# Kernel optimization log

Measured on AMD Instinct MI355X. Metric: run time of the kernel, lower is better.

## Reference

```python
import jax, jax.numpy as jnp
import numpy as np

N, E, IN, HID, HEADS, L = 50000, 640000, 32, 64, 2, 4
MAXR = 8
N_ETYPE = 11 + 3 * MAXR  # 35
NEG_SLOPE = 0.2  # DGL EGATConv leaky_relu slope


def _mlp2(x, W1, b1, W2, b2):
    # 2-layer MLP: activation (gelu) after hidden layer only
    return jax.nn.gelu(x @ W1 + b1) @ W2 + b2


def _egat(h, ef, src, dst, W_ni, W_nj, W_fij, W_node, b_node, attn):
    # DGL EGATConv: edge-feature-enhanced graph attention
    n = h.shape[0]
    H, D = attn.shape
    f_edge = (h @ W_ni)[src] + (h @ W_nj)[dst] + ef @ W_fij       # [E, H*D]
    f_out = jax.nn.leaky_relu(f_edge, NEG_SLOPE).reshape(-1, H, D)
    e = jnp.einsum('ehd,hd->eh', f_out, attn)                     # [E, H]
    m = jax.ops.segment_max(e, dst, num_segments=n)               # per-dst max
    w = jnp.exp(e - m[dst])
    z = jax.ops.segment_sum(w, dst, num_segments=n)
    a = w / z[dst]                                                # edge softmax over incoming edges
    h_out = (h @ W_node + b_node).reshape(n, H, D)
    return jax.ops.segment_sum(h_out[src] * a[:, :, None], dst, num_segments=n)  # [N, H, D]


def _forward(feat, att_rc, att_rp, type_emb, rid_emb, rc_W, rc_b, rp_W, rp_b,
             fe_W1, fe_b1, fe_W2, fe_b2, W_ni, W_nj, W_fij, W_node, b_node, attn,
             mlp_W1, mlp_b1, mlp_W2, mlp_b2, src, dst, etype, erid):
    n = feat.shape[0]
    # edge embedding, 'sum' flavor
    ef = type_emb[etype] + rid_emb[erid] + att_rc @ rc_W + rc_b + att_rp @ rp_W + rp_b
    feats = [feat]
    h = _mlp2(feat, fe_W1, fe_b1, fe_W2, fe_b2)
    feats.append(h)
    for l in range(W_ni.shape[0]):
        agg = _egat(h, ef, src, dst, W_ni[l], W_nj[l], W_fij[l],
                    W_node[l], b_node[l], attn[l])
        h = _mlp2(agg.reshape(n, -1), mlp_W1[l], mlp_b1[l], mlp_W2[l], mlp_b2[l]) + h  # residual
        feats.append(h)
    node_emb = jnp.concatenate(feats, axis=-1)             # layer_pooling='all'
    graph_emb = jnp.max(node_emb, axis=0, keepdims=True)   # graph max pooling
    return jnp.concatenate([node_emb, jnp.broadcast_to(graph_emb, node_emb.shape)], axis=-1)


def setup_inputs() -> dict:
    key = jax.random.key(0)
    ks = iter(jax.random.split(key, 40))
    s = 0.05
    return {
        'feat': jax.random.normal(next(ks), (N, IN), jnp.float32),
        'att_rc': jax.random.normal(next(ks), (E, 2), jnp.float32),
        'att_rp': jax.random.normal(next(ks), (E, 3), jnp.float32),
        'type_emb': jax.random.normal(next(ks), (N_ETYPE, HID), jnp.float32) * s,
        'rid_emb': jax.random.normal(next(ks), (MAXR + 1, HID), jnp.float32) * s,
        'rc_W': jax.random.normal(next(ks), (2, HID), jnp.float32) * s,
        'rc_b': jnp.zeros((HID,), jnp.float32),
        'rp_W': jax.random.normal(next(ks), (3, HID), jnp.float32) * s,
        'rp_b': jnp.zeros((HID,), jnp.float32),
        'fe_W1': jax.random.normal(next(ks), (IN, HID), jnp.float32) * s,
        'fe_b1': jnp.zeros((HID,), jnp.float32),
        'fe_W2': jax.random.normal(next(ks), (HID, HID), jnp.float32) * s,
        'fe_b2': jnp.zeros((HID,), jnp.float32),
        'W_ni': jax.random.normal(next(ks), (L, HID, HEADS * HID), jnp.float32) * s,
        'W_nj': jax.random.normal(next(ks), (L, HID, HEADS * HID), jnp.float32) * s,
        'W_fij': jax.random.normal(next(ks), (L, HID, HEADS * HID), jnp.float32) * s,
        'W_node': jax.random.normal(next(ks), (L, HID, HEADS * HID), jnp.float32) * s,
        'b_node': jnp.zeros((L, HEADS * HID), jnp.float32),
        'attn': jax.random.normal(next(ks), (L, HEADS, HID), jnp.float32) * s,
        'mlp_W1': jax.random.normal(next(ks), (L, HEADS * HID, HEADS * HID), jnp.float32) * s,
        'mlp_b1': jnp.zeros((L, HEADS * HID), jnp.float32),
        'mlp_W2': jax.random.normal(next(ks), (L, HEADS * HID, HID), jnp.float32) * s,
        'mlp_b2': jnp.zeros((L, HID), jnp.float32),
        'src': jax.random.randint(next(ks), (E,), 0, N, jnp.int32),
        'dst': jax.random.randint(next(ks), (E,), 0, N, jnp.int32),
        'etype': jax.random.randint(next(ks), (E,), 0, N_ETYPE, jnp.int32),
        'erid': jax.random.randint(next(ks), (E,), 0, MAXR + 1, jnp.int32),
    }


def reference(feat, att_rc, att_rp, type_emb, rid_emb, rc_W, rc_b, rp_W, rp_b,
              fe_W1, fe_b1, fe_W2, fe_b2, W_ni, W_nj, W_fij, W_node, b_node, attn,
              mlp_W1, mlp_b1, mlp_W2, mlp_b2, src, dst, etype, erid):
    return _forward(feat, att_rc, att_rp, type_emb, rid_emb, rc_W, rc_b, rp_W, rp_b,
                    fe_W1, fe_b1, fe_W2, fe_b2, W_ni, W_nj, W_fij, W_node, b_node, attn,
                    mlp_W1, mlp_b1, mlp_W2, mlp_b2, src, dst, etype, erid)
```

## Files before the change

kernel.cpp:

```cpp
#include <hip/hip_runtime.h>
#include <math.h>

#define N_NODES 50000
#define N_EDGES 640000
#define NLAYER  4
#define NPAD    50016

typedef unsigned short bf16_t;
typedef __attribute__((ext_vector_type(8))) short s16x8;
typedef __attribute__((ext_vector_type(4))) float f32x4;

__device__ __forceinline__ float gelu_f(float x) {
    return 0.5f * x * (1.0f + tanhf(0.7978845608028654f * (x + 0.044715f * x * x * x)));
}

__device__ __forceinline__ bf16_t f2bf(float f) {
    unsigned u = __float_as_uint(f);
    unsigned r = (u + 0x7FFFu + ((u >> 16) & 1u)) >> 16;
    return (bf16_t)r;
}
__device__ __forceinline__ float bf2f(bf16_t h) { return __uint_as_float(((unsigned)h) << 16); }
__device__ __forceinline__ float bfl(unsigned x) { return __uint_as_float(x << 16); }
__device__ __forceinline__ float bfh(unsigned x) { return __uint_as_float(x & 0xFFFF0000u); }

__global__ void k_zero32(unsigned* p, int n) {
    int i = blockIdx.x * 256 + threadIdx.x;
    if (i < n) p[i] = 0u;
}

__global__ void k_hist(const int* __restrict__ dst, int* __restrict__ deg) {
    int i = blockIdx.x * 256 + threadIdx.x;
    if (i < N_EDGES) atomicAdd(&deg[dst[i]], 1);
}

__global__ void k_scan1(const int* __restrict__ deg, int* __restrict__ rowptr, int* __restrict__ bsum) {
    __shared__ int sd[1024];
    int gi = blockIdx.x * 1024 + threadIdx.x;
    int v = (gi < N_NODES) ? deg[gi] : 0;
    sd[threadIdx.x] = v;
    __syncthreads();
    for (int off = 1; off < 1024; off <<= 1) {
        int t2 = (threadIdx.x >= (unsigned)off) ? sd[threadIdx.x - off] : 0;
        __syncthreads();
        sd[threadIdx.x] += t2;
        __syncthreads();
    }
    if (gi < N_NODES) rowptr[gi] = sd[threadIdx.x] - v;
    if (threadIdx.x == 1023) bsum[blockIdx.x] = sd[1023];
}

__global__ void k_scan2(const int* __restrict__ bsum, int* __restrict__ boff, int nb) {
    if (threadIdx.x == 0 && blockIdx.x == 0) {
        int run = 0;
        for (int b = 0; b < nb; b++) { boff[b] = run; run += bsum[b]; }
    }
}

__global__ void k_scan3(int* __restrict__ rowptr, const int* __restrict__ boff) {
    int gi = blockIdx.x * 1024 + threadIdx.x;
    if (gi < N_NODES) rowptr[gi] += boff[blockIdx.x];
    if (gi == 0) rowptr[N_NODES] = N_EDGES;
}

__global__ void k_copy(const int* __restrict__ a, int* __restrict__ b) {
    int i = blockIdx.x * 256 + threadIdx.x;
    if (i < N_NODES) b[i] = a[i];
}

__global__ void k_scatter(const int* __restrict__ dst, int* __restrict__ cursor, int* __restrict__ eidx) {
    int i = blockIdx.x * 256 + threadIdx.x;
    if (i < N_EDGES) {
        int p = atomicAdd(&cursor[dst[i]], 1);
        eidx[p] = i;
    }
}

__global__ void k_sortgather(
    const int* __restrict__ eidx, const int* __restrict__ src, const int* __restrict__ dst,
    const int* __restrict__ etype, const int* __restrict__ erid,
    const float* __restrict__ att_rc, const float* __restrict__ att_rp,
    int* __restrict__ src_s, int* __restrict__ dst_s,
    int* __restrict__ etype_s, int* __restrict__ erid_s,
    float* __restrict__ rc_s, float* __restrict__ rp_s)
{
    int i = blockIdx.x * 256 + threadIdx.x;
    if (i < N_EDGES) {
        int e = eidx[i];
        src_s[i] = src[e];
        dst_s[i] = dst[e];
        etype_s[i] = etype[e];
        erid_s[i] = erid[e];
        rc_s[2 * i] = att_rc[2 * e];
        rc_s[2 * i + 1] = att_rc[2 * e + 1];
        rp_s[3 * i] = att_rp[3 * e];
        rp_s[3 * i + 1] = att_rp[3 * e + 1];
        rp_s[3 * i + 2] = att_rp[3 * e + 2];
    }
}

__global__ void k_wprep(const float* __restrict__ Wfij, const float* __restrict__ Wni,
                        const float* __restrict__ Wnj, const float* __restrict__ Wnode,
                        const float* __restrict__ W1, const float* __restrict__ W2,
                        bf16_t* __restrict__ WT, bf16_t* __restrict__ W3T,
                        bf16_t* __restrict__ W1T, bf16_t* __restrict__ W2T)
{
    int idx = blockIdx.x * 256 + threadIdx.x;
    if (idx >= NLAYER * 57344) return;
    int l = idx / 57344, r = idx % 57344;
    if (r < 8192) {
        int n = r >> 6, k = r & 63;
        WT[l * 8192 + r] = f2bf(Wfij[l * 8192 + k * 128 + n]);
    } else if (r < 32768) {
        int q = r - 8192; int c = q >> 6, k = q & 63;
        const float* src = (c < 128) ? Wni : (c < 256) ? Wnj : Wnode;
        W3T[l * 24576 + q] = f2bf(src[l * 8192 + k * 128 + (c & 127)]);
    } else if (r < 49152) {
        int q = r - 32768; int n = q >> 7, k = q & 127;
        W1T[l * 16384 + q] = f2bf(W1[l * 16384 + k * 128 + n]);
    } else {
        int q = r - 49152; int j = q >> 7, k = q & 127;
        W2T[l * 8192 + q] = f2bf(W2[l * 8192 + k * 64 + j]);
    }
}

__global__ __launch_bounds__(256) void k_fe(
    const float* __restrict__ feat, const float* __restrict__ W1, const float* __restrict__ b1,
    const float* __restrict__ W2, const float* __restrict__ b2,
    float* __restrict__ h, bf16_t* __restrict__ hb, float* __restrict__ out)
{
    __shared__ float hid[4][64];
    int w = threadIdx.x >> 6, lane = threadIdx.x & 63;
    int n = blockIdx.x * 4 + w;
    float a = b1[lane];
#pragma unroll 8
    for (int k = 0; k < 32; k++) a = fmaf(feat[n * 32 + k], W1[k * 64 + lane], a);
    hid[w][lane] = gelu_f(a);
    __syncthreads();
    float o = b2[lane];
#pragma unroll 8
    for (int k = 0; k < 64; k++) o = fmaf(hid[w][k], W2[k * 64 + lane], o);
    h[n * 64 + lane] = o;
    hb[n * 64 + lane] = f2bf(o);
    out[n * 704 + 32 + lane] = o;
    if (lane < 32) out[n * 704 + lane] = feat[n * 32 + lane];
}

__global__ __launch_bounds__(256) void k_node3(
    const bf16_t* __restrict__ hb, const bf16_t* __restrict__ W3T,
    const float* __restrict__ bnode, bf16_t* __restrict__ s)
{
    __shared__ __align__(16) bf16_t hbS[32 * 72];
    const int t = threadIdx.x;
    const int wave = t >> 6, lane = t & 63, l16 = lane & 15, quad = lane >> 4;
    const int n0 = blockIdx.x * 32;
    {
        int r = t >> 3, sg = t & 7;
        *(s16x8*)(hbS + r * 72 + sg * 8) = *(const s16x8*)(hb + (size_t)(n0 + r) * 64 + sg * 8);
    }
    __syncthreads();
    const int ng = wave & 1, ch = wave >> 1;
    const s16x8 B0 = *(const s16x8*)(hbS + (ng * 16 + l16) * 72 + quad * 8);
    const s16x8 B1 = *(const s16x8*)(hbS + (ng * 16 + l16) * 72 + 32 + quad * 8);
    const int node = n0 + ng * 16 + l16;
#pragma unroll
    for (int nt = 0; nt < 12; nt++) {
        int c0 = ch * 192 + nt * 16;
        const s16x8 A0 = *(const s16x8*)(W3T + (size_t)(c0 + l16) * 64 + quad * 8);
        const s16x8 A1 = *(const s16x8*)(W3T + (size_t)(c0 + l16) * 64 + 32 + quad * 8);
        f32x4 acc = {0.f, 0.f, 0.f, 0.f};
        acc = __builtin_amdgcn_mfma_f32_16x16x32_bf16(A0, B0, acc, 0, 0, 0);
        acc = __builtin_amdgcn_mfma_f32_16x16x32_bf16(A1, B1, acc, 0, 0, 0);
        int cb = c0 + quad * 4;
        float4 bv = make_float4(0.f, 0.f, 0.f, 0.f);
        if (cb >= 256) bv = *(const float4*)(bnode + cb - 256);
        ushort4 o;
        o.x = f2bf(acc[0] + bv.x);
        o.y = f2bf(acc[1] + bv.y);
        o.z = f2bf(acc[2] + bv.z);
        o.w = f2bf(acc[3] + bv.w);
        *(ushort4*)(s + (size_t)node * 384 + cb) = o;
    }
}

__global__ __launch_bounds__(256) void k_edge(
    const bf16_t* __restrict__ s, const bf16_t* __restrict__ WT,
    const float* __restrict__ attn,
    const float* __restrict__ type_emb, const float* __restrict__ rid_emb,
    const float* __restrict__ rcW, const float* __restrict__ rcb,
    const float* __restrict__ rpW, const float* __restrict__ rpb,
    const float* __restrict__ rc_s, const float* __restrict__ rp_s,
    const int* __restrict__ etype_s, const int* __restrict__ erid_s,
    const int* __restrict__ src_s, const int* __restrict__ dst_s,
    float* __restrict__ evals)
{
    __shared__ __align__(16) bf16_t efA[32 * 72];
    __shared__ __align__(16) bf16_t SND[32 * 136];
    const int t = threadIdx.x;
    const int wave = t >> 6, lane = t & 63;
    const int l16 = lane & 15, quad = lane >> 4;
    const int eg = wave & 1, head = wave >> 1;

    s16x8 Aw[4][2];
    float4 att4[4];
#pragma unroll
    for (int mt = 0; mt < 4; mt++) {
        const bf16_t* wrow = WT + (head * 64 + mt * 16 + l16) * 64 + quad * 8;
        Aw[mt][0] = *(const s16x8*)(wrow);
        Aw[mt][1] = *(const s16x8*)(wrow + 32);
        att4[mt] = *(const float4*)(attn + head * 64 + mt * 16 + quad * 4);
    }

    for (int tile = blockIdx.x; tile < N_EDGES / 32; tile += gridDim.x) {
        const int eb = tile * 32;
        __syncthreads();
        {
            int e = t & 31, kg = (t >> 5) * 8;
            int i = eb + e;
            int et = etype_s[i] * 64, er = erid_s[i] * 64;
            float rc0 = rc_s[i * 2 + 0], rc1 = rc_s[i * 2 + 1];
            float rp0 = rp_s[i * 3 + 0], rp1 = rp_s[i * 3 + 1], rp2 = rp_s[i * 3 + 2];
            bf16_t tmp[8];
#pragma unroll
            for (int kk = 0; kk < 8; kk++) {
                int k = kg + kk;
                float v = type_emb[et + k] + rid_emb[er + k] + rcb[k] + rpb[k];
                v = fmaf(rc0, rcW[k], v);
                v = fmaf(rc1, rcW[64 + k], v);
                v = fmaf(rp0, rpW[k], v);
                v = fmaf(rp1, rpW[64 + k], v);
                v = fmaf(rp2, rpW[128 + k], v);
                tmp[kk] = f2bf(v);
            }
            *(s16x8*)(&efA[e * 72 + kg]) = *(const s16x8*)tmp;
        }
        {
#pragma unroll
            for (int j = 0; j < 2; j++) {
                int c = t * 2 + j;
                int e = c >> 4, p = c & 15;
                int i = eb + e;
                const uint4 U = *(const uint4*)(s + (size_t)src_s[i] * 384 + p * 8);
                const uint4 V = *(const uint4*)(s + (size_t)dst_s[i] * 384 + 128 + p * 8);
                bf16_t o[8];
                o[0] = f2bf(bfl(U.x) + bfl(V.x)); o[1] = f2bf(bfh(U.x) + bfh(V.x));
                o[2] = f2bf(bfl(U.y) + bfl(V.y)); o[3] = f2bf(bfh(U.y) + bfh(V.y));
                o[4] = f2bf(bfl(U.z) + bfl(V.z)); o[5] = f2bf(bfh(U.z) + bfh(V.z));
                o[6] = f2bf(bfl(U.w) + bfl(V.w)); o[7] = f2bf(bfh(U.w) + bfh(V.w));
                *(s16x8*)(&SND[e * 136 + p * 8]) = *(const s16x8*)o;
            }
        }
        __syncthreads();

        const int e = eg * 16 + l16;
        const s16x8 B0 = *(const s16x8*)(&efA[e * 72 + quad * 8]);
        const s16x8 B1 = *(const s16x8*)(&efA[e * 72 + 32 + quad * 8]);
        f32x4 acc[4];
#pragma unroll
        for (int mt = 0; mt < 4; mt++) {
            f32x4 a = {0.f, 0.f, 0.f, 0.f};
            a = __builtin_amdgcn_mfma_f32_16x16x32_bf16(Aw[mt][0], B0, a, 0, 0, 0);
            a = __builtin_amdgcn_mfma_f32_16x16x32_bf16(Aw[mt][1], B1, a, 0, 0, 0);
            acc[mt] = a;
        }

        float p = 0.f;
#pragma unroll
        for (int mt = 0; mt < 4; mt++) {
            const ushort4 sv = *(const ushort4*)(&SND[e * 136 + mt * 16 + quad * 4]);
            float f0 = acc[mt][0] + bf2f(sv.x);
            float f1 = acc[mt][1] + bf2f(sv.y);
            float f2 = acc[mt][2] + bf2f(sv.z);
            float f3 = acc[mt][3] + bf2f(sv.w);
            f0 = (f0 >= 0.f) ? f0 : 0.2f * f0;
            f1 = (f1 >= 0.f) ? f1 : 0.2f * f1;
            f2 = (f2 >= 0.f) ? f2 : 0.2f * f2;
            f3 = (f3 >= 0.f) ? f3 : 0.2f * f3;
            p = fmaf(f0, att4[mt].x, p);
            p = fmaf(f1, att4[mt].y, p);
            p = fmaf(f2, att4[mt].z, p);
            p = fmaf(f3, att4[mt].w, p);
        }
        p += __shfl_xor(p, 16);
        p += __shfl_xor(p, 32);
        if (quad == 0) evals[(eb + e) * 2 + head] = p;
    }
}

__global__ __launch_bounds__(256) void k_soft_agg(
    const int* __restrict__ rowptr, const int* __restrict__ src_s,
    const float* __restrict__ evals, const bf16_t* __restrict__ s,
    unsigned* __restrict__ aggb)
{
    int lane = threadIdx.x & 63;
    int wid = (blockIdx.x * 256 + threadIdx.x) >> 6;
    int nw = (gridDim.x * 256) >> 6;
    const int h1 = (lane >= 32) ? 1 : 0;
    const int half = lane & 31;
    for (int n = wid; n < N_NODES; n += nw) {
        int r0 = rowptr[n], r1 = rowptr[n + 1];
        unsigned* aout = aggb + (size_t)n * 64 + lane;
        if (r0 == r1) { *aout = 0u; continue; }
        float mm = -1e30f;
        for (int i = r0 + half; i < r1; i += 32) mm = fmaxf(mm, evals[2 * i + h1]);
#pragma unroll
        for (int off = 1; off < 32; off <<= 1) mm = fmaxf(mm, __shfl_xor(mm, off));
        float z = 0.f;
        for (int i = r0 + half; i < r1; i += 32) z += expf(evals[2 * i + h1] - mm);
#pragma unroll
        for (int off = 1; off < 32; off <<= 1) z += __shfl_xor(z, off);
        float rz = 1.f / z;
        float acc0 = 0.f, acc1 = 0.f;
        for (int i = r0; i < r1; i += 8) {
            int cnt = r1 - i;
            unsigned cc[8]; float ww[8];
#pragma unroll
            for (int j = 0; j < 8; j++) {
                if (j < cnt) {
                    cc[j] = *(const unsigned*)(s + (size_t)src_s[i + j] * 384 + 256 + 2 * lane);
                    ww[j] = expf(evals[2 * (i + j) + h1] - mm) * rz;
                } else { cc[j] = 0u; ww[j] = 0.f; }
            }
#pragma unroll
            for (int j = 0; j < 8; j++) {
                acc0 = fmaf(ww[j], bfl(cc[j]), acc0);
                acc1 = fmaf(ww[j], bfh(cc[j]), acc1);
            }
        }
        *aout = (unsigned)f2bf(acc0) | ((unsigned)f2bf(acc1) << 16);
    }
}

__global__ __launch_bounds__(256) void k_mlp(
    const bf16_t* __restrict__ aggb, const bf16_t* __restrict__ W1T, const float* __restrict__ b1,
    const bf16_t* __restrict__ W2T, const float* __restrict__ b2,
    const float* __restrict__ hin, float* __restrict__ hout, bf16_t* __restrict__ houtb,
    float* __restrict__ out, int col0)
{
    __shared__ __align__(16) bf16_t aggS[32 * 136];
    __shared__ __align__(16) bf16_t hidS[32 * 136];
    const int t = threadIdx.x;
    const int wave = t >> 6, lane = t & 63, l16 = lane & 15, quad = lane >> 4;
    const int n0 = blockIdx.x * 32;
    {
        int r = t >> 3, sg = t & 7;
        *(s16x8*)(aggS + r * 136 + sg * 16) =
            *(const s16x8*)(aggb + (size_t)(n0 + r) * 128 + sg * 16);
        *(s16x8*)(aggS + r * 136 + sg * 16 + 8) =
            *(const s16x8*)(aggb + (size_t)(n0 + r) * 128 + sg * 16 + 8);
    }
    __syncthreads();
    const int ng = wave & 1, nh = wave >> 1;
    const int node = n0 + ng * 16 + l16;
    {
        const bf16_t* brow = aggS + (ng * 16 + l16) * 136 + quad * 8;
        s16x8 B[4];
#pragma unroll
        for (int ks = 0; ks < 4; ks++) B[ks] = *(const s16x8*)(brow + ks * 32);
#pragma unroll
        for (int nt = 0; nt < 4; nt++) {
            int nb = nh * 64 + nt * 16;
            f32x4 acc = {0.f, 0.f, 0.f, 0.f};
#pragma unroll
            for (int ks = 0; ks < 4; ks++) {
                const s16x8 A = *(const s16x8*)(W1T + (size_t)(nb + l16) * 128 + ks * 32 + quad * 8);
                acc = __builtin_amdgcn_mfma_f32_16x16x32_bf16(A, B[ks], acc, 0, 0, 0);
            }
            const float4 bv = *(const float4*)(b1 + nb + quad * 4);
            ushort4 o;
            o.x = f2bf(gelu_f(acc[0] + bv.x));
            o.y = f2bf(gelu_f(acc[1] + bv.y));
            o.z = f2bf(gelu_f(acc[2] + bv.z));
            o.w = f2bf(gelu_f(acc[3] + bv.w));
            *(ushort4*)(hidS + (ng * 16 + l16) * 136 + nb + quad * 4) = o;
        }
    }
    __syncthreads();
    {
        const int jh = wave >> 1;
        const bf16_t* hrow = hidS + (ng * 16 + l16) * 136 + quad * 8;
        s16x8 H[4];
#pragma unroll
        for (int ks = 0; ks < 4; ks++) H[ks] = *(const s16x8*)(hrow + ks * 32);
#pragma unroll
        for (int jt = 0; jt < 2; jt++) {
            int jb = jh * 32 + jt * 16;
            f32x4 acc = {0.f, 0.f, 0.f, 0.f};
#pragma unroll
            for (int ks = 0; ks < 4; ks++) {
                const s16x8 A = *(const s16x8*)(W2T + (size_t)(jb + l16) * 128 + ks * 32 + quad * 8);
                acc = __builtin_amdgcn_mfma_f32_16x16x32_bf16(A, H[ks], acc, 0, 0, 0);
            }
            int j0 = jb + quad * 4;
            const float4 bv = *(const float4*)(b2 + j0);
            const float4 hv = *(const float4*)(hin + (size_t)node * 64 + j0);
            float4 v;
            v.x = acc[0] + bv.x + hv.x;
            v.y = acc[1] + bv.y + hv.y;
            v.z = acc[2] + bv.z + hv.z;
            v.w = acc[3] + bv.w + hv.w;
            *(float4*)(hout + (size_t)node * 64 + j0) = v;
            ushort4 ob;
            ob.x = f2bf(v.x); ob.y = f2bf(v.y); ob.z = f2bf(v.z); ob.w = f2bf(v.w);
            *(ushort4*)(houtb + (size_t)node * 64 + j0) = ob;
            if (node < N_NODES)
                *(float4*)(out + (size_t)node * 704 + col0 + j0) = v;
        }
    }
}

__device__ __forceinline__ unsigned fmap(float v) {
    unsigned u = __float_as_uint(v);
    return (u & 0x80000000u) ? ~u : (u | 0x80000000u);
}

__global__ __launch_bounds__(384) void k_colmax(const float* __restrict__ out, unsigned* __restrict__ gmax) {
    int c = threadIdx.x;
    if (c >= 352) return;
    float m = -1e30f;
    for (int n = blockIdx.x; n < N_NODES; n += gridDim.x)
        m = fmaxf(m, out[(size_t)n * 704 + c]);
    atomicMax(gmax + c, fmap(m));
}

__global__ __launch_bounds__(384) void k_bcast(const unsigned* __restrict__ gmax, float* __restrict__ out) {
    int c = threadIdx.x;
    if (c >= 352) return;
    unsigned u = gmax[c];
    u = (u & 0x80000000u) ? (u ^ 0x80000000u) : ~u;
    float v = __uint_as_float(u);
    for (int n = blockIdx.x; n < N_NODES; n += gridDim.x)
        out[(size_t)n * 704 + 352 + c] = v;
}

extern "C" void kernel_launch(void* const* d_in, const int* in_sizes, int n_in,
                              void* d_out, int out_size, void* d_ws, size_t ws_size,
                              hipStream_t stream)
{
    (void)in_sizes; (void)n_in; (void)out_size; (void)ws_size;
    const float* feat     = (const float*)d_in[0];
    const float* att_rc   = (const float*)d_in[1];
    const float* att_rp   = (const float*)d_in[2];
    const float* type_emb = (const float*)d_in[3];
    const float* rid_emb  = (const float*)d_in[4];
    const float* rc_W     = (const float*)d_in[5];
    const float* rc_b     = (const float*)d_in[6];
    const float* rp_W     = (const float*)d_in[7];
    const float* rp_b     = (const float*)d_in[8];
    const float* fe_W1    = (const float*)d_in[9];
    const float* fe_b1    = (const float*)d_in[10];
    const float* fe_W2    = (const float*)d_in[11];
    const float* fe_b2    = (const float*)d_in[12];
    const float* W_ni     = (const float*)d_in[13];
    const float* W_nj     = (const float*)d_in[14];
    const float* W_fij    = (const float*)d_in[15];
    const float* W_node   = (const float*)d_in[16];
    const float* b_node   = (const float*)d_in[17];
    const float* attn     = (const float*)d_in[18];
    const float* mlp_W1   = (const float*)d_in[19];
    const float* mlp_b1   = (const float*)d_in[20];
    const float* mlp_W2   = (const float*)d_in[21];
    const float* mlp_b2   = (const float*)d_in[22];
    const int* src   = (const int*)d_in[23];
    const int* dst   = (const int*)d_in[24];
    const int* etype = (const int*)d_in[25];
    const int* erid  = (const int*)d_in[26];
    float* out = (float*)d_out;

    char* cur = (char*)d_ws;
    auto alloc = [&](size_t bytes) { char* p = cur; cur += (bytes + 15) & ~(size_t)15; return p; };
    float* h_a    = (float*)alloc((size_t)NPAD * 64 * 4);
    float* h_b    = (float*)alloc((size_t)NPAD * 64 * 4);
    bf16_t* hb_a  = (bf16_t*)alloc((size_t)NPAD * 64 * 2);
    bf16_t* hb_b  = (bf16_t*)alloc((size_t)NPAD * 64 * 2);
    bf16_t* s     = (bf16_t*)alloc((size_t)NPAD * 384 * 2);
    float* ev     = (float*)alloc((size_t)N_EDGES * 2 * 4);
    bf16_t* aggb  = (bf16_t*)alloc((size_t)NPAD * 128 * 2);
    int* deg     = (int*)alloc((size_t)N_NODES * 4);
    int* rowptr  = (int*)alloc((size_t)(N_NODES + 1) * 4);
    int* cursor  = (int*)alloc((size_t)N_NODES * 4);
    int* eidx    = (int*)alloc((size_t)N_EDGES * 4);
    int* src_s   = (int*)alloc((size_t)N_EDGES * 4);
    int* dst_s   = (int*)alloc((size_t)N_EDGES * 4);
    int* etype_s = (int*)alloc((size_t)N_EDGES * 4);
    int* erid_s  = (int*)alloc((size_t)N_EDGES * 4);
    float* rc_s  = (float*)alloc((size_t)N_EDGES * 2 * 4);
    float* rp_s  = (float*)alloc((size_t)N_EDGES * 3 * 4);
    bf16_t* WT   = (bf16_t*)alloc((size_t)NLAYER * 128 * 64 * 2);
    bf16_t* W3T  = (bf16_t*)alloc((size_t)NLAYER * 384 * 64 * 2);
    bf16_t* W1T  = (bf16_t*)alloc((size_t)NLAYER * 128 * 128 * 2);
    bf16_t* W2T  = (bf16_t*)alloc((size_t)NLAYER * 64 * 128 * 2);
    int* bsum    = (int*)alloc(64 * 4);
    int* boff    = (int*)alloc(64 * 4);
    unsigned* gmax = (unsigned*)alloc(352 * 4);

    const int NB = (N_NODES + 1023) / 1024;

    k_zero32<<<(N_NODES + 255) / 256, 256, 0, stream>>>((unsigned*)deg, N_NODES);
    k_zero32<<<2, 256, 0, stream>>>(gmax, 352);
    k_hist<<<N_EDGES / 256, 256, 0, stream>>>(dst, deg);
    k_scan1<<<NB, 1024, 0, stream>>>(deg, rowptr, bsum);
    k_scan2<<<1, 64, 0, stream>>>(bsum, boff, NB);
    k_scan3<<<NB, 1024, 0, stream>>>(rowptr, boff);
    k_copy<<<(N_NODES + 255) / 256, 256, 0, stream>>>(rowptr, cursor);
    k_scatter<<<N_EDGES / 256, 256, 0, stream>>>(dst, cursor, eidx);
    k_sortgather<<<N_EDGES / 256, 256, 0, stream>>>(eidx, src, dst, etype, erid, att_rc, att_rp,
                                                    src_s, dst_s, etype_s, erid_s, rc_s, rp_s);
    k_wprep<<<(NLAYER * 57344 + 255) / 256, 256, 0, stream>>>(
        W_fij, W_ni, W_nj, W_node, mlp_W1, mlp_W2, WT, W3T, W1T, W2T);
    k_fe<<<N_NODES / 4, 256, 0, stream>>>(feat, fe_W1, fe_b1, fe_W2, fe_b2, h_a, hb_a, out);

    float* hc = h_a;  bf16_t* hbc = hb_a;
    float* hn = h_b;  bf16_t* hbn = hb_b;
    for (int l = 0; l < NLAYER; l++) {
        k_node3<<<NPAD / 32, 256, 0, stream>>>(hbc, W3T + (size_t)l * 384 * 64, b_node + l * 128, s);
        k_edge<<<2560, 256, 0, stream>>>(s, WT + l * 128 * 64, attn + l * 128,
                                         type_emb, rid_emb, rc_W, rc_b, rp_W, rp_b,
                                         rc_s, rp_s, etype_s, erid_s, src_s, dst_s, ev);
        k_soft_agg<<<4096, 256, 0, stream>>>(rowptr, src_s, ev, s, (unsigned*)aggb);
        k_mlp<<<NPAD / 32, 256, 0, stream>>>(aggb, W1T + (size_t)l * 128 * 128, mlp_b1 + l * 128,
                                             W2T + (size_t)l * 64 * 128, mlp_b2 + l * 64,
                                             hc, hn, hbn, out, 32 + 64 * (l + 1));
        float* tf = hc; hc = hn; hn = tf;
        bf16_t* tb = hbc; hbc = hbn; hbn = tb;
    }
    k_colmax<<<512, 384, 0, stream>>>(out, gmax);
    k_bcast<<<512, 384, 0, stream>>>(gmax, out);
}
```

Baseline: 1.330 ms.

## Restructure edge kernel to per-wave tiles with packed edge metadata and base table

Packs per-edge metadata (combined type/rid index, src, dst, rc/rp attributes) into a 32-byte record so the edge kernel does two vector loads per edge instead of many scattered ones. Precomputes a 315x64 table of type+rid embeddings plus biases, which removes two embedding lookups and bias adds per edge. The edge kernel now has each wave process 16 edges for both heads directly from registers, with weights staged once in LDS, removing per-tile block barriers and the LDS round trips. This raises register pressure (both heads' weight fragments held in registers) and each wave's gathers of node rows are narrower.

```diff
diff --git a/kernel.cpp b/kernel.cpp
--- a/kernel.cpp
+++ b/kernel.cpp
@@ -79,23 +79,36 @@
     const int* __restrict__ eidx, const int* __restrict__ src, const int* __restrict__ dst,
     const int* __restrict__ etype, const int* __restrict__ erid,
     const float* __restrict__ att_rc, const float* __restrict__ att_rp,
-    int* __restrict__ src_s, int* __restrict__ dst_s,
-    int* __restrict__ etype_s, int* __restrict__ erid_s,
-    float* __restrict__ rc_s, float* __restrict__ rp_s)
+    int* __restrict__ src_s, uint4* __restrict__ emeta)
 {
     int i = blockIdx.x * 256 + threadIdx.x;
     if (i < N_EDGES) {
         int e = eidx[i];
-        src_s[i] = src[e];
-        dst_s[i] = dst[e];
-        etype_s[i] = etype[e];
-        erid_s[i] = erid[e];
-        rc_s[2 * i] = att_rc[2 * e];
-        rc_s[2 * i + 1] = att_rc[2 * e + 1];
-        rp_s[3 * i] = att_rp[3 * e];
-        rp_s[3 * i + 1] = att_rp[3 * e + 1];
-        rp_s[3 * i + 2] = att_rp[3 * e + 2];
-    }
+        int sv = src[e];
+        src_s[i] = sv;
+        uint4 a, b;
+        a.x = (unsigned)(etype[e] * 9 + erid[e]);
+        a.y = (unsigned)sv;
+        a.z = (unsigned)dst[e];
+        a.w = __float_as_uint(att_rc[2 * e]);
+        b.x = __float_as_uint(att_rc[2 * e + 1]);
+        b.y = __float_as_uint(att_rp[3 * e]);
+        b.z = __float_as_uint(att_rp[3 * e + 1]);
+        b.w = __float_as_uint(att_rp[3 * e + 2]);
+        emeta[2 * i] = a;
+        emeta[2 * i + 1] = b;
+    }
+}
+
+__global__ void k_base(const float* __restrict__ type_emb, const float* __restrict__ rid_emb,
+                       const float* __restrict__ rcb, const float* __restrict__ rpb,
+                       float* __restrict__ base)
+{
+    int idx = blockIdx.x * 256 + threadIdx.x;
+    if (idx >= 315 * 64) return;
+    int c = idx >> 6, k = idx & 63;
+    int et = c / 9, er = c % 9;
+    base[idx] = type_emb[et * 64 + k] + rid_emb[er * 64 + k] + rcb[k] + rpb[k];
 }
 
 __global__ void k_wprep(const float* __restrict__ Wfij, const float* __restrict__ Wni,
@@ -184,105 +197,123 @@
 
 __global__ __launch_bounds__(256) void k_edge(
     const bf16_t* __restrict__ s, const bf16_t* __restrict__ WT,
-    const float* __restrict__ attn,
-    const float* __restrict__ type_emb, const float* __restrict__ rid_emb,
-    const float* __restrict__ rcW, const float* __restrict__ rcb,
-    const float* __restrict__ rpW, const float* __restrict__ rpb,
-    const float* __restrict__ rc_s, const float* __restrict__ rp_s,
-    const int* __restrict__ etype_s, const int* __restrict__ erid_s,
-    const int* __restrict__ src_s, const int* __restrict__ dst_s,
-    float* __restrict__ evals)
-{
-    __shared__ __align__(16) bf16_t efA[32 * 72];
-    __shared__ __align__(16) bf16_t SND[32 * 136];
-    const int t = threadIdx.x;
-    const int wave = t >> 6, lane = t & 63;
+    const float* __restrict__ attn, const uint4* __restrict__ emeta,
+    const float* __restrict__ base, const float* __restrict__ rcW,
+    const float* __restrict__ rpW, float* __restrict__ evals)
+{
+    __shared__ __align__(16) bf16_t WTl[128 * 72];
+    __shared__ __align__(16) float attL[128];
+    __shared__ __align__(16) float cwL[5][64];
+    for (int c = threadIdx.x; c < 1024; c += 256) {
+        int r = c >> 3, q = c & 7;
+        *(s16x8*)(WTl + r * 72 + q * 8) = *(const s16x8*)(WT + r * 64 + q * 8);
+    }
+    if (threadIdx.x < 128) attL[threadIdx.x] = attn[threadIdx.x];
+    {
+        int j = threadIdx.x >> 6, k = threadIdx.x & 63;
+        cwL[j][k] = (j < 2) ? rcW[j * 64 + k] : rpW[(j - 2) * 64 + k];
+        if (threadIdx.x < 64) cwL[4][threadIdx.x] = rpW[128 + threadIdx.x];
+    }
+    __syncthreads();
+
+    const int lane = threadIdx.x & 63;
     const int l16 = lane & 15, quad = lane >> 4;
-    const int eg = wave & 1, head = wave >> 1;
-
-    s16x8 Aw[4][2];
-    float4 att4[4];
-#pragma unroll
-    for (int mt = 0; mt < 4; mt++) {
-        const bf16_t* wrow = WT + (head * 64 + mt * 16 + l16) * 64 + quad * 8;
-        Aw[mt][0] = *(const s16x8*)(wrow);
-        Aw[mt][1] = *(const s16x8*)(wrow + 32);
-        att4[mt] = *(const float4*)(attn + head * 64 + mt * 16 + quad * 4);
-    }
-
-    for (int tile = blockIdx.x; tile < N_EDGES / 32; tile += gridDim.x) {
-        const int eb = tile * 32;
-        __syncthreads();
-        {
-            int e = t & 31, kg = (t >> 5) * 8;
-            int i = eb + e;
-            int et = etype_s[i] * 64, er = erid_s[i] * 64;
-            float rc0 = rc_s[i * 2 + 0], rc1 = rc_s[i * 2 + 1];
-            float rp0 = rp_s[i * 3 + 0], rp1 = rp_s[i * 3 + 1], rp2 = rp_s[i * 3 + 2];
-            bf16_t tmp[8];
-#pragma unroll
-            for (int kk = 0; kk < 8; kk++) {
-                int k = kg + kk;
-                float v = type_emb[et + k] + rid_emb[er + k] + rcb[k] + rpb[k];
-                v = fmaf(rc0, rcW[k], v);
-                v = fmaf(rc1, rcW[64 + k], v);
-                v = fmaf(rp0, rpW[k], v);
-                v = fmaf(rp1, rpW[64 + k], v);
-                v = fmaf(rp2, rpW[128 + k], v);
-                tmp[kk] = f2bf(v);
+
+    s16x8 Aw[2][4][2];
+#pragma unroll
+    for (int hd = 0; hd < 2; hd++)
+#pragma unroll
+        for (int mt = 0; mt < 4; mt++) {
+            const bf16_t* arow = WTl + (hd * 64 + mt * 16 + l16) * 72 + quad * 8;
+            Aw[hd][mt][0] = *(const s16x8*)(arow);
+            Aw[hd][mt][1] = *(const s16x8*)(arow + 32);
+        }
+
+    const int nw = (gridDim.x * 256) >> 6;
+    for (int tile = (blockIdx.x * 256 + threadIdx.x) >> 6; tile < N_EDGES / 16; tile += nw) {
+        const int i = tile * 16 + l16;
+        const uint4 m0 = emeta[2 * i];
+        const uint4 m1 = emeta[2 * i + 1];
+
+        const bf16_t* srow = s + (size_t)m0.y * 384;
+        const bf16_t* drow = s + (size_t)m0.z * 384 + 128;
+        ushort4 niv[4], njv[4];
+#pragma unroll
+        for (int mt = 0; mt < 4; mt++) {
+            const int d0 = mt * 16 + quad * 4;
+            niv[mt] = *(const ushort4*)(srow + d0);
+            njv[mt] = *(const ushort4*)(drow + d0);
+        }
+
+        const float* bp = base + (size_t)m0.x * 64;
+        const float4 bv0 = *(const float4*)(bp + quad * 8);
+        const float4 bv1 = *(const float4*)(bp + quad * 8 + 4);
+        const float4 bv2 = *(const float4*)(bp + 32 + quad * 8);
+        const float4 bv3 = *(const float4*)(bp + 32 + quad * 8 + 4);
+        const float rc0 = __uint_as_float(m0.w), rc1 = __uint_as_float(m1.x);
+        const float rp0 = __uint_as_float(m1.y), rp1 = __uint_as_float(m1.z), rp2 = __uint_as_float(m1.w);
+
+        auto efg = [&](const float4& bv, int k) -> ushort4 {
+            const float4 w0 = *(const float4*)(&cwL[0][k]);
+            const float4 w1 = *(const float4*)(&cwL[1][k]);
+            const float4 w2 = *(const float4*)(&cwL[2][k]);
+            const float4 w3 = *(const float4*)(&cwL[3][k]);
+            const float4 w4 = *(const float4*)(&cwL[4][k]);
+            float v0 = bv.x, v1 = bv.y, v2 = bv.z, v3 = bv.w;
+            v0 = fmaf(rc0, w0.x, v0); v1 = fmaf(rc0, w0.y, v1); v2 = fmaf(rc0, w0.z, v2); v3 = fmaf(rc0, w0.w, v3);
+            v0 = fmaf(rc1, w1.x, v0); v1 = fmaf(rc1, w1.y, v1); v2 = fmaf(rc1, w1.z, v2); v3 = fmaf(rc1, w1.w, v3);
+            v0 = fmaf(rp0, w2.x, v0); v1 = fmaf(rp0, w2.y, v1); v2 = fmaf(rp0, w2.z, v2); v3 = fmaf(rp0, w2.w, v3);
+            v0 = fmaf(rp1, w3.x, v0); v1 = fmaf(rp1, w3.y, v1); v2 = fmaf(rp1, w3.z, v2); v3 = fmaf(rp1, w3.w, v3);
+            v0 = fmaf(rp2, w4.x, v0); v1 = fmaf(rp2, w4.y, v1); v2 = fmaf(rp2, w4.z, v2); v3 = fmaf(rp2, w4.w, v3);
+            ushort4 r;
+            r.x = f2bf(v0); r.y = f2bf(v1); r.z = f2bf(v2); r.w = f2bf(v3);
+            return r;
+        };
+        const ushort4 e0 = efg(bv0, quad * 8);
+        const ushort4 e1 = efg(bv1, quad * 8 + 4);
+        const ushort4 e2 = efg(bv2, 32 + quad * 8);
+        const ushort4 e3 = efg(bv3, 32 + quad * 8 + 4);
+        s16x8 B0, B1;
+        B0[0] = (short)e0.x; B0[1] = (short)e0.y; B0[2] = (short)e0.z; B0[3] = (short)e0.w;
+        B0[4] = (short)e1.x; B0[5] = (short)e1.y; B0[6] = (short)e1.z; B0[7] = (short)e1.w;
+        B1[0] = (short)e2.x; B1[1] = (short)e2.y; B1[2] = (short)e2.z; B1[3] = (short)e2.w;
+        B1[4] = (short)e3.x; B1[5] = (short)e3.y; B1[6] = (short)e3.z; B1[7] = (short)e3.w;
+
+        ushort4 snd[4];
+#pragma unroll
+        for (int mt = 0; mt < 4; mt++) {
+            snd[mt].x = f2bf(bf2f(niv[mt].x) + bf2f(njv[mt].x));
+            snd[mt].y = f2bf(bf2f(niv[mt].y) + bf2f(njv[mt].y));
+            snd[mt].z = f2bf(bf2f(niv[mt].z) + bf2f(njv[mt].z));
+            snd[mt].w = f2bf(bf2f(niv[mt].w) + bf2f(njv[mt].w));
+        }
+
+#pragma unroll
+        for (int hd = 0; hd < 2; hd++) {
+            float p = 0.f;
+#pragma unroll
+            for (int mt = 0; mt < 4; mt++) {
+                f32x4 a = {0.f, 0.f, 0.f, 0.f};
+                a = __builtin_amdgcn_mfma_f32_16x16x32_bf16(Aw[hd][mt][0], B0, a, 0, 0, 0);
+                a = __builtin_amdgcn_mfma_f32_16x16x32_bf16(Aw[hd][mt][1], B1, a, 0, 0, 0);
+                const float4 at = *(const float4*)(attL + hd * 64 + mt * 16 + quad * 4);
+                float f0 = a[0] + bf2f(snd[mt].x);
+                float f1 = a[1] + bf2f(snd[mt].y);
+                float f2 = a[2] + bf2f(snd[mt].z);
+                float f3 = a[3] + bf2f(snd[mt].w);
+                f0 = (f0 >= 0.f) ? f0 : 0.2f * f0;
+                f1 = (f1 >= 0.f) ? f1 : 0.2f * f1;
+                f2 = (f2 >= 0.f) ? f2 : 0.2f * f2;
+                f3 = (f3 >= 0.f) ? f3 : 0.2f * f3;
+                p = fmaf(f0, at.x, p);
+                p = fmaf(f1, at.y, p);
+                p = fmaf(f2, at.z, p);
+                p = fmaf(f3, at.w, p);
             }
-            *(s16x8*)(&efA[e * 72 + kg]) = *(const s16x8*)tmp;
-        }
-        {
-#pragma unroll
-            for (int j = 0; j < 2; j++) {
-                int c = t * 2 + j;
-                int e = c >> 4, p = c & 15;
-                int i = eb + e;
-                const uint4 U = *(const uint4*)(s + (size_t)src_s[i] * 384 + p * 8);
-                const uint4 V = *(const uint4*)(s + (size_t)dst_s[i] * 384 + 128 + p * 8);
-                bf16_t o[8];
-                o[0] = f2bf(bfl(U.x) + bfl(V.x)); o[1] = f2bf(bfh(U.x) + bfh(V.x));
-                o[2] = f2bf(bfl(U.y) + bfl(V.y)); o[3] = f2bf(bfh(U.y) + bfh(V.y));
-                o[4] = f2bf(bfl(U.z) + bfl(V.z)); o[5] = f2bf(bfh(U.z) + bfh(V.z));
-                o[6] = f2bf(bfl(U.w) + bfl(V.w)); o[7] = f2bf(bfh(U.w) + bfh(V.w));
-                *(s16x8*)(&SND[e * 136 + p * 8]) = *(const s16x8*)o;
-            }
-        }
-        __syncthreads();
-
-        const int e = eg * 16 + l16;
-        const s16x8 B0 = *(const s16x8*)(&efA[e * 72 + quad * 8]);
-        const s16x8 B1 = *(const s16x8*)(&efA[e * 72 + 32 + quad * 8]);
-        f32x4 acc[4];
-#pragma unroll
-        for (int mt = 0; mt < 4; mt++) {
-            f32x4 a = {0.f, 0.f, 0.f, 0.f};
-            a = __builtin_amdgcn_mfma_f32_16x16x32_bf16(Aw[mt][0], B0, a, 0, 0, 0);
-            a = __builtin_amdgcn_mfma_f32_16x16x32_bf16(Aw[mt][1], B1, a, 0, 0, 0);
-            acc[mt] = a;
-        }
-
-        float p = 0.f;
-#pragma unroll
-        for (int mt = 0; mt < 4; mt++) {
-            const ushort4 sv = *(const ushort4*)(&SND[e * 136 + mt * 16 + quad * 4]);
-            float f0 = acc[mt][0] + bf2f(sv.x);
-            float f1 = acc[mt][1] + bf2f(sv.y);
-            float f2 = acc[mt][2] + bf2f(sv.z);
-            float f3 = acc[mt][3] + bf2f(sv.w);
-            f0 = (f0 >= 0.f) ? f0 : 0.2f * f0;
-            f1 = (f1 >= 0.f) ? f1 : 0.2f * f1;
-            f2 = (f2 >= 0.f) ? f2 : 0.2f * f2;
-            f3 = (f3 >= 0.f) ? f3 : 0.2f * f3;
-            p = fmaf(f0, att4[mt].x, p);
-            p = fmaf(f1, att4[mt].y, p);
-            p = fmaf(f2, att4[mt].z, p);
-            p = fmaf(f3, att4[mt].w, p);
-        }
-        p += __shfl_xor(p, 16);
-        p += __shfl_xor(p, 32);
-        if (quad == 0) evals[(eb + e) * 2 + head] = p;
+            p += __shfl_xor(p, 16);
+            p += __shfl_xor(p, 32);
+            if (quad == 0) evals[i * 2 + hd] = p;
+        }
     }
 }
 
@@ -480,11 +511,8 @@
     int* cursor  = (int*)alloc((size_t)N_NODES * 4);
     int* eidx    = (int*)alloc((size_t)N_EDGES * 4);
     int* src_s   = (int*)alloc((size_t)N_EDGES * 4);
-    int* dst_s   = (int*)alloc((size_t)N_EDGES * 4);
-    int* etype_s = (int*)alloc((size_t)N_EDGES * 4);
-    int* erid_s  = (int*)alloc((size_t)N_EDGES * 4);
-    float* rc_s  = (float*)alloc((size_t)N_EDGES * 2 * 4);
-    float* rp_s  = (float*)alloc((size_t)N_EDGES * 3 * 4);
+    uint4* emeta = (uint4*)alloc((size_t)N_EDGES * 32);
+    float* baseT = (float*)alloc((size_t)315 * 64 * 4);
     bf16_t* WT   = (bf16_t*)alloc((size_t)NLAYER * 128 * 64 * 2);
     bf16_t* W3T  = (bf16_t*)alloc((size_t)NLAYER * 384 * 64 * 2);
     bf16_t* W1T  = (bf16_t*)alloc((size_t)NLAYER * 128 * 128 * 2);
@@ -504,7 +532,8 @@
     k_copy<<<(N_NODES + 255) / 256, 256, 0, stream>>>(rowptr, cursor);
     k_scatter<<<N_EDGES / 256, 256, 0, stream>>>(dst, cursor, eidx);
     k_sortgather<<<N_EDGES / 256, 256, 0, stream>>>(eidx, src, dst, etype, erid, att_rc, att_rp,
-                                                    src_s, dst_s, etype_s, erid_s, rc_s, rp_s);
+                                                    src_s, emeta);
+    k_base<<<(315 * 64 + 255) / 256, 256, 0, stream>>>(type_emb, rid_emb, rc_b, rp_b, baseT);
     k_wprep<<<(NLAYER * 57344 + 255) / 256, 256, 0, stream>>>(
         W_fij, W_ni, W_nj, W_node, mlp_W1, mlp_W2, WT, W3T, W1T, W2T);
     k_fe<<<N_NODES / 4, 256, 0, stream>>>(feat, fe_W1, fe_b1, fe_W2, fe_b2, h_a, hb_a, out);
@@ -513,9 +542,8 @@
     float* hn = h_b;  bf16_t* hbn = hb_b;
     for (int l = 0; l < NLAYER; l++) {
         k_node3<<<NPAD / 32, 256, 0, stream>>>(hbc, W3T + (size_t)l * 384 * 64, b_node + l * 128, s);
-        k_edge<<<2560, 256, 0, stream>>>(s, WT + l * 128 * 64, attn + l * 128,
-                                         type_emb, rid_emb, rc_W, rc_b, rp_W, rp_b,
-                                         rc_s, rp_s, etype_s, erid_s, src_s, dst_s, ev);
+        k_edge<<<2560, 256, 0, stream>>>(s, WT + l * 128 * 64, attn + l * 128, emeta, baseT,
+                                         rc_W, rp_W, ev);
         k_soft_agg<<<4096, 256, 0, stream>>>(rowptr, src_s, ev, s, (unsigned*)aggb);
         k_mlp<<<NPAD / 32, 256, 0, stream>>>(aggb, W1T + (size_t)l * 128 * 128, mlp_b1 + l * 128,
                                              W2T + (size_t)l * 64 * 128, mlp_b2 + l * 64,
```

Measured after the change: 1.136 ms. 1.17x faster.
